# Kernel optimization log

Measured on AMD Instinct MI355X. Metric: run time of the kernel, lower is better.

Reference implementation:

```python
import jax, jax.numpy as jnp
import numpy as np

MACRO_CURVE_ORDER = 3
MAX_ACTION_LEN = 24
NUM_CURVES = 8
VOCAB = 361
NUM_LAYERS = 6
HID = 32


def setup_inputs() -> dict:
    key = jax.random.key(0)
    ks = iter(jax.random.split(key, 32))
    B, N_PART, P, CTX = 4096, 100, 64, 64

    def lin(k, din, dout):
        k1, k2 = jax.random.split(k)
        s = 1.0 / np.sqrt(din)
        return (jax.random.uniform(k1, (din, dout), jnp.float32, -s, s),
                jax.random.uniform(k2, (dout,), jnp.float32, -s, s))

    fc1_w, fc1_b = lin(next(ks), P, 256)
    fc2_w, fc2_b = lin(next(ks), 256, 256)
    fc3_w, fc3_b = lin(next(ks), CTX + 256, 512)
    fc4_w, fc4_b = lin(next(ks), 512, 256)
    fc5_w, fc5_b = lin(next(ks), 256, 128)
    fc6_w, fc6_b = lin(next(ks), 128, 32)
    fc10_w, fc10_b = lin(next(ks), HID, VOCAB)

    s = 1.0 / np.sqrt(HID)
    lstm_wih = jax.random.uniform(next(ks), (NUM_LAYERS, HID, 4 * HID), jnp.float32, -s, s)
    lstm_whh = jax.random.uniform(next(ks), (NUM_LAYERS, HID, 4 * HID), jnp.float32, -s, s)
    lstm_bih = jax.random.uniform(next(ks), (NUM_LAYERS, 4 * HID), jnp.float32, -s, s)
    lstm_bhh = jax.random.uniform(next(ks), (NUM_LAYERS, 4 * HID), jnp.float32, -s, s)

    return {
        "c": jax.random.normal(next(ks), (B, CTX), jnp.float32),
        "x": jax.random.normal(next(ks), (B, N_PART * P), jnp.float32),
        "hidden": jnp.zeros((NUM_LAYERS, B, HID), jnp.float32),
        "cell": jnp.zeros((NUM_LAYERS, B, HID), jnp.float32),
        "fc1_w": fc1_w, "fc1_b": fc1_b, "fc2_w": fc2_w, "fc2_b": fc2_b,
        "fc3_w": fc3_w, "fc3_b": fc3_b, "fc4_w": fc4_w, "fc4_b": fc4_b,
        "fc5_w": fc5_w, "fc5_b": fc5_b, "fc6_w": fc6_w, "fc6_b": fc6_b,
        "lstm_wih": lstm_wih, "lstm_whh": lstm_whh,
        "lstm_bih": lstm_bih, "lstm_bhh": lstm_bhh,
        "fc10_w": fc10_w, "fc10_b": fc10_b,
        "particle_size": P,
    }


def _lstm_stack(x, h, c, wih, whh, bih, bhh):
    """One time step through 6 stacked LSTM layers (PyTorch cell math)."""
    hs, cs = [], []
    inp = x
    for l in range(NUM_LAYERS):
        gates = inp @ wih[l] + bih[l] + h[l] @ whh[l] + bhh[l]  # (B, 4*HID)
        i, f, g, o = jnp.split(gates, 4, axis=-1)
        i, f, o = jax.nn.sigmoid(i), jax.nn.sigmoid(f), jax.nn.sigmoid(o)
        g = jnp.tanh(g)
        c_new = f * c[l] + i * g
        h_new = o * jnp.tanh(c_new)
        hs.append(h_new)
        cs.append(c_new)
        inp = h_new
    return inp, jnp.stack(hs), jnp.stack(cs)


def reference(c, x, hidden, cell, fc1_w, fc1_b, fc2_w, fc2_b, fc3_w, fc3_b,
              fc4_w, fc4_b, fc5_w, fc5_b, fc6_w, fc6_b,
              lstm_wih, lstm_whh, lstm_bih, lstm_bhh, fc10_w, fc10_b,
              particle_size):
    B = x.shape[0]
    # Belief (particle) encoder with mean pooling.
    xp = x.reshape(B, -1, particle_size)
    xp = jax.nn.relu(xp @ fc1_w + fc1_b)
    xp = jax.nn.relu(xp @ fc2_w + fc2_b)
    xp = xp.mean(axis=-2)  # (B, 256)
    z = jnp.concatenate([c, xp], axis=-1)
    z = jax.nn.relu(z @ fc3_w + fc3_b)
    z = jax.nn.relu(z @ fc4_w + fc4_b)
    z = jax.nn.relu(z @ fc5_w + fc5_b)
    z = jax.nn.relu(z @ fc6_w + fc6_b)  # (B, 32)

    def step(carry, _):
        xt, h, cst = carry
        xt, h, cst = _lstm_stack(xt, h, cst, lstm_wih, lstm_whh, lstm_bih, lstm_bhh)
        logits = xt @ fc10_w + fc10_b  # (B, VOCAB)
        idx = jax.lax.top_k(logits, NUM_CURVES)[1]  # (B, NUM_CURVES)
        return (xt, h, cst), idx

    (_, _, _), idxs = jax.lax.scan(step, (z, hidden, cell), None, length=MAX_ACTION_LEN)
    # (T, B, K) -> (B, T*K)
    preds = jnp.transpose(idxs, (1, 0, 2)).reshape(B, MAX_ACTION_LEN * NUM_CURVES)
    return preds
```

## Files before the change

### kernel.cpp

```cpp
#include <hip/hip_runtime.h>
#include <math.h>

#define BATCH 4096
#define NPART 100
#define PSZ   64

__global__ __launch_bounds__(256, 3) void k_encoder(
    const float* __restrict__ x,
    const float* __restrict__ w1, const float* __restrict__ b1,
    const float* __restrict__ w2, const float* __restrict__ b2,
    float* __restrict__ xp)
{
    __shared__ float h1[32][256];
    const int tid = threadIdx.x;
    const int b   = blockIdx.x;

    float w1c[64];
    #pragma unroll
    for (int k = 0; k < 64; ++k) w1c[k] = w1[k * 256 + tid];
    const float b1j = b1[tid];

    const int tx = tid & 31;
    const int ty = tid >> 5;
    const float4 b2a = *(const float4*)&b2[tx * 8];
    const float4 b2b = *(const float4*)&b2[tx * 8 + 4];
    float msum[8] = {0.f,0.f,0.f,0.f,0.f,0.f,0.f,0.f};

    const float* xb  = x + (size_t)b * (NPART * PSZ);
    const float* w2p = w2 + tx * 8;

    for (int ch = 0; ch < 4; ++ch) {
        const int rbase = ch * 32;
        const int rows  = (rbase + 32 <= NPART) ? 32 : (NPART - rbase);

        #pragma unroll 2
        for (int p = 0; p < rows; ++p) {
            const float4* xr = (const float4*)(xb + (rbase + p) * 64);
            float acc = b1j;
            #pragma unroll
            for (int kq = 0; kq < 16; ++kq) {
                const float4 xv = xr[kq];
                acc = fmaf(xv.x, w1c[4*kq+0], acc);
                acc = fmaf(xv.y, w1c[4*kq+1], acc);
                acc = fmaf(xv.z, w1c[4*kq+2], acc);
                acc = fmaf(xv.w, w1c[4*kq+3], acc);
            }
            h1[p][tid] = fmaxf(acc, 0.f);
        }
        __syncthreads();

        float acc[4][8];
        #pragma unroll
        for (int r = 0; r < 4; ++r)
            #pragma unroll
            for (int q = 0; q < 8; ++q) acc[r][q] = 0.f;

        #pragma unroll 2
        for (int k0 = 0; k0 < 256; k0 += 4) {
            float4 bv0[4], bv1[4];
            #pragma unroll
            for (int kk = 0; kk < 4; ++kk) {
                bv0[kk] = *(const float4*)(w2p + (k0 + kk) * 256);
                bv1[kk] = *(const float4*)(w2p + (k0 + kk) * 256 + 4);
            }
            float4 av[4];
            #pragma unroll
            for (int r = 0; r < 4; ++r)
                av[r] = *(const float4*)&h1[ty * 4 + r][k0];
            #pragma unroll
            for (int r = 0; r < 4; ++r) {
                const float a0 = av[r].x, a1 = av[r].y, a2 = av[r].z, a3 = av[r].w;
                acc[r][0] = fmaf(a0, bv0[0].x, fmaf(a1, bv0[1].x, fmaf(a2, bv0[2].x, fmaf(a3, bv0[3].x, acc[r][0]))));
                acc[r][1] = fmaf(a0, bv0[0].y, fmaf(a1, bv0[1].y, fmaf(a2, bv0[2].y, fmaf(a3, bv0[3].y, acc[r][1]))));
                acc[r][2] = fmaf(a0, bv0[0].z, fmaf(a1, bv0[1].z, fmaf(a2, bv0[2].z, fmaf(a3, bv0[3].z, acc[r][2]))));
                acc[r][3] = fmaf(a0, bv0[0].w, fmaf(a1, bv0[1].w, fmaf(a2, bv0[2].w, fmaf(a3, bv0[3].w, acc[r][3]))));
                acc[r][4] = fmaf(a0, bv1[0].x, fmaf(a1, bv1[1].x, fmaf(a2, bv1[2].x, fmaf(a3, bv1[3].x, acc[r][4]))));
                acc[r][5] = fmaf(a0, bv1[0].y, fmaf(a1, bv1[1].y, fmaf(a2, bv1[2].y, fmaf(a3, bv1[3].y, acc[r][5]))));
                acc[r][6] = fmaf(a0, bv1[0].z, fmaf(a1, bv1[1].z, fmaf(a2, bv1[2].z, fmaf(a3, bv1[3].z, acc[r][6]))));
                acc[r][7] = fmaf(a0, bv1[0].w, fmaf(a1, bv1[1].w, fmaf(a2, bv1[2].w, fmaf(a3, bv1[3].w, acc[r][7]))));
            }
        }

        #pragma unroll
        for (int r = 0; r < 4; ++r) {
            const int grow = rbase + ty * 4 + r;
            if (grow < NPART) {
                msum[0] += fmaxf(acc[r][0] + b2a.x, 0.f);
                msum[1] += fmaxf(acc[r][1] + b2a.y, 0.f);
                msum[2] += fmaxf(acc[r][2] + b2a.z, 0.f);
                msum[3] += fmaxf(acc[r][3] + b2a.w, 0.f);
                msum[4] += fmaxf(acc[r][4] + b2b.x, 0.f);
                msum[5] += fmaxf(acc[r][5] + b2b.y, 0.f);
                msum[6] += fmaxf(acc[r][6] + b2b.z, 0.f);
                msum[7] += fmaxf(acc[r][7] + b2b.w, 0.f);
            }
        }
        __syncthreads();
    }

    float* red = &h1[0][0];
    #pragma unroll
    for (int q = 0; q < 8; ++q) red[ty * 256 + tx * 8 + q] = msum[q];
    __syncthreads();
    float s = 0.f;
    #pragma unroll
    for (int g = 0; g < 8; ++g) s += red[g * 256 + tid];
    xp[(size_t)b * 256 + tid] = s / 100.0f;
}

__global__ __launch_bounds__(256) void k_mlp(
    const float* __restrict__ cin, const float* __restrict__ xp,
    const float* __restrict__ w3, const float* __restrict__ b3,
    const float* __restrict__ w4, const float* __restrict__ b4,
    const float* __restrict__ w5, const float* __restrict__ b5,
    const float* __restrict__ w6, const float* __restrict__ b6,
    float* __restrict__ z)
{
    __shared__ float in0[8][320];
    __shared__ float h3[8][512];
    __shared__ float h4[8][256];
    __shared__ float h5[8][128];
    const int tid  = threadIdx.x;
    const int row0 = blockIdx.x * 8;

    for (int i = tid; i < 8 * 16; i += 256) {
        int r = i >> 4, q = i & 15;
        *(float4*)&in0[r][q * 4] = *(const float4*)&cin[(size_t)(row0 + r) * 64 + q * 4];
    }
    for (int i = tid; i < 8 * 64; i += 256) {
        int r = i >> 6, q = i & 63;
        *(float4*)&in0[r][64 + q * 4] = *(const float4*)&xp[(size_t)(row0 + r) * 256 + q * 4];
    }
    __syncthreads();

    {
        float a0[8], a1[8];
        #pragma unroll
        for (int r = 0; r < 8; ++r) { a0[r] = 0.f; a1[r] = 0.f; }
        const int c0 = tid, c1 = tid + 256;
        for (int kq = 0; kq < 80; ++kq) {
            const int k0 = kq * 4;
            float wa0 = w3[(k0+0)*512 + c0], wa1 = w3[(k0+1)*512 + c0];
            float wa2 = w3[(k0+2)*512 + c0], wa3 = w3[(k0+3)*512 + c0];
            float wb0 = w3[(k0+0)*512 + c1], wb1 = w3[(k0+1)*512 + c1];
            float wb2 = w3[(k0+2)*512 + c1], wb3 = w3[(k0+3)*512 + c1];
            #pragma unroll
            for (int r = 0; r < 8; ++r) {
                const float4 a = *(const float4*)&in0[r][k0];
                a0[r] = fmaf(a.x, wa0, fmaf(a.y, wa1, fmaf(a.z, wa2, fmaf(a.w, wa3, a0[r]))));
                a1[r] = fmaf(a.x, wb0, fmaf(a.y, wb1, fmaf(a.z, wb2, fmaf(a.w, wb3, a1[r]))));
            }
        }
        const float bb0 = b3[c0], bb1 = b3[c1];
        #pragma unroll
        for (int r = 0; r < 8; ++r) {
            h3[r][c0] = fmaxf(a0[r] + bb0, 0.f);
            h3[r][c1] = fmaxf(a1[r] + bb1, 0.f);
        }
    }
    __syncthreads();

    {
        float ac[8];
        #pragma unroll
        for (int r = 0; r < 8; ++r) ac[r] = 0.f;
        for (int kq = 0; kq < 128; ++kq) {
            const int k0 = kq * 4;
            float w0 = w4[(k0+0)*256 + tid], w1v = w4[(k0+1)*256 + tid];
            float w2v = w4[(k0+2)*256 + tid], w3v = w4[(k0+3)*256 + tid];
            #pragma unroll
            for (int r = 0; r < 8; ++r) {
                const float4 a = *(const float4*)&h3[r][k0];
                ac[r] = fmaf(a.x, w0, fmaf(a.y, w1v, fmaf(a.z, w2v, fmaf(a.w, w3v, ac[r]))));
            }
        }
        const float bb = b4[tid];
        #pragma unroll
        for (int r = 0; r < 8; ++r) h4[r][tid] = fmaxf(ac[r] + bb, 0.f);
    }
    __syncthreads();

    {
        const int c5 = tid & 127, half = tid >> 7;
        float ac[4];
        #pragma unroll
        for (int r = 0; r < 4; ++r) ac[r] = 0.f;
        for (int kq = 0; kq < 64; ++kq) {
            const int k0 = kq * 4;
            float w0 = w5[(k0+0)*128 + c5], w1v = w5[(k0+1)*128 + c5];
            float w2v = w5[(k0+2)*128 + c5], w3v = w5[(k0+3)*128 + c5];
            #pragma unroll
            for (int r = 0; r < 4; ++r) {
                const float4 a = *(const float4*)&h4[half * 4 + r][k0];
                ac[r] = fmaf(a.x, w0, fmaf(a.y, w1v, fmaf(a.z, w2v, fmaf(a.w, w3v, ac[r]))));
            }
        }
        const float bb = b5[c5];
        #pragma unroll
        for (int r = 0; r < 4; ++r) h5[half * 4 + r][c5] = fmaxf(ac[r] + bb, 0.f);
    }
    __syncthreads();

    {
        const int c6 = tid & 31, r = tid >> 5;
        float ac = 0.f;
        for (int kq = 0; kq < 32; ++kq) {
            const int k0 = kq * 4;
            float w0 = w6[(k0+0)*32 + c6], w1v = w6[(k0+1)*32 + c6];
            float w2v = w6[(k0+2)*32 + c6], w3v = w6[(k0+3)*32 + c6];
            const float4 a = *(const float4*)&h5[r][k0];
            ac = fmaf(a.x, w0, fmaf(a.y, w1v, fmaf(a.z, w2v, fmaf(a.w, w3v, ac))));
        }
        z[(size_t)(row0 + r) * 32 + c6] = fmaxf(ac + b6[c6], 0.f);
    }
}

__global__ __launch_bounds__(256) void k_lstm(
    const float* __restrict__ z,
    const float* __restrict__ hid0, const float* __restrict__ cel0,
    const float* __restrict__ wih, const float* __restrict__ whh,
    const float* __restrict__ bih, const float* __restrict__ bhh,
    const float* __restrict__ w10, const float* __restrict__ b10,
    int* __restrict__ out)
{
    __shared__ float xs[8][32];
    __shared__ float hs[6][8][32];
    __shared__ float cs[6][8][32];
    __shared__ float gates[8][128];
    __shared__ float logits[8][361];
    const int tid  = threadIdx.x;
    const int row0 = blockIdx.x * 8;

    for (int i = tid; i < 8 * 32; i += 256) xs[0][i] = z[(size_t)row0 * 32 + i];
    for (int i = tid; i < 6 * 8 * 32; i += 256) {
        int l = i >> 8, rj = i & 255;
        (&hs[0][0][0])[i] = hid0[(size_t)l * BATCH * 32 + (size_t)row0 * 32 + rj];
        (&cs[0][0][0])[i] = cel0[(size_t)l * BATCH * 32 + (size_t)row0 * 32 + rj];
    }
    __syncthreads();

    const int g  = tid & 127, rg = tid >> 7;
    const int jc = tid & 31,  jr = tid >> 5;
    const int wv = tid >> 6,  lane = tid & 63;

    for (int t = 0; t < 24; ++t) {
        for (int l = 0; l < 6; ++l) {
            const float* inp = (l == 0) ? ((t == 0) ? &xs[0][0] : &hs[5][0][0])
                                        : &hs[l - 1][0][0];
            const float* WI = wih + (size_t)l * 32 * 128;
            const float* WH = whh + (size_t)l * 32 * 128;
            const float bsum = bih[l * 128 + g] + bhh[l * 128 + g];
            float acc[4] = {bsum, bsum, bsum, bsum};
            #pragma unroll
            for (int k = 0; k < 32; k += 4) {
                float wi0 = WI[(k+0)*128 + g], wi1 = WI[(k+1)*128 + g];
                float wi2 = WI[(k+2)*128 + g], wi3 = WI[(k+3)*128 + g];
                float wh0 = WH[(k+0)*128 + g], wh1 = WH[(k+1)*128 + g];
                float wh2 = WH[(k+2)*128 + g], wh3 = WH[(k+3)*128 + g];
                #pragma unroll
                for (int rr = 0; rr < 4; ++rr) {
                    const int r = rg * 4 + rr;
                    const float4 ai = *(const float4*)&inp[r * 32 + k];
                    const float4 ah = *(const float4*)&hs[l][r][k];
                    acc[rr] = fmaf(ai.x, wi0, acc[rr]); acc[rr] = fmaf(ai.y, wi1, acc[rr]);
                    acc[rr] = fmaf(ai.z, wi2, acc[rr]); acc[rr] = fmaf(ai.w, wi3, acc[rr]);
                    acc[rr] = fmaf(ah.x, wh0, acc[rr]); acc[rr] = fmaf(ah.y, wh1, acc[rr]);
                    acc[rr] = fmaf(ah.z, wh2, acc[rr]); acc[rr] = fmaf(ah.w, wh3, acc[rr]);
                }
            }
            #pragma unroll
            for (int rr = 0; rr < 4; ++rr) gates[rg * 4 + rr][g] = acc[rr];
            __syncthreads();

            {
                const float gi = gates[jr][jc],      gf = gates[jr][32 + jc];
                const float gg = gates[jr][64 + jc], go = gates[jr][96 + jc];
                const float i_ = 1.f / (1.f + expf(-gi));
                const float f_ = 1.f / (1.f + expf(-gf));
                const float o_ = 1.f / (1.f + expf(-go));
                const float g_ = tanhf(gg);
                const float cn = f_ * cs[l][jr][jc] + i_ * g_;
                cs[l][jr][jc] = cn;
                hs[l][jr][jc] = o_ * tanhf(cn);
            }
            __syncthreads();
        }

        #pragma unroll
        for (int pass = 0; pass < 2; ++pass) {
            const int v = tid + pass * 256;
            if (v < 361) {
                const float bb = b10[v];
                float a8[8];
                #pragma unroll
                for (int r = 0; r < 8; ++r) a8[r] = bb;
                #pragma unroll
                for (int k = 0; k < 32; k += 4) {
                    float w0 = w10[(k+0)*361 + v], w1v = w10[(k+1)*361 + v];
                    float w2v = w10[(k+2)*361 + v], w3v = w10[(k+3)*361 + v];
                    #pragma unroll
                    for (int r = 0; r < 8; ++r) {
                        const float4 a = *(const float4*)&hs[5][r][k];
                        a8[r] = fmaf(a.x, w0, fmaf(a.y, w1v, fmaf(a.z, w2v, fmaf(a.w, w3v, a8[r]))));
                    }
                }
                #pragma unroll
                for (int r = 0; r < 8; ++r) logits[r][v] = a8[r];
            }
        }
        __syncthreads();

        for (int rr = 0; rr < 2; ++rr) {
            const int r = wv * 2 + rr;
            float val[6];
            #pragma unroll
            for (int s = 0; s < 6; ++s) {
                const int v = lane + 64 * s;
                val[s] = (v < 361) ? logits[r][v] : -3.4e38f;
            }
            unsigned msk = 0x3Fu;
            const int rowg = row0 + r;
            for (int sel = 0; sel < 8; ++sel) {
                float bv = -3.4e38f; int bi = 0x7FFFFFFF;
                #pragma unroll
                for (int s = 0; s < 6; ++s) {
                    if (msk & (1u << s)) {
                        const float v2 = val[s]; const int i2 = lane + 64 * s;
                        if (v2 > bv || (v2 == bv && i2 < bi)) { bv = v2; bi = i2; }
                    }
                }
                #pragma unroll
                for (int off = 32; off >= 1; off >>= 1) {
                    const float ov = __shfl_xor(bv, off, 64);
                    const int   oi = __shfl_xor(bi, off, 64);
                    if (ov > bv || (ov == bv && oi < bi)) { bv = ov; bi = oi; }
                }
                if ((bi & 63) == lane) msk &= ~(1u << (bi >> 6));
                if (lane == 0) out[(size_t)rowg * 192 + t * 8 + sel] = bi;
            }
        }
        __syncthreads();
    }
}

extern "C" void kernel_launch(void* const* d_in, const int* in_sizes, int n_in,
                              void* d_out, int out_size, void* d_ws, size_t ws_size,
                              hipStream_t stream) {
    const float* cin  = (const float*)d_in[0];
    const float* x    = (const float*)d_in[1];
    const float* hid0 = (const float*)d_in[2];
    const float* cel0 = (const float*)d_in[3];
    const float* w1 = (const float*)d_in[4];  const float* b1 = (const float*)d_in[5];
    const float* w2 = (const float*)d_in[6];  const float* b2 = (const float*)d_in[7];
    const float* w3 = (const float*)d_in[8];  const float* b3 = (const float*)d_in[9];
    const float* w4 = (const float*)d_in[10]; const float* b4 = (const float*)d_in[11];
    const float* w5 = (const float*)d_in[12]; const float* b5 = (const float*)d_in[13];
    const float* w6 = (const float*)d_in[14]; const float* b6 = (const float*)d_in[15];
    const float* wih = (const float*)d_in[16]; const float* whh = (const float*)d_in[17];
    const float* bih = (const float*)d_in[18]; const float* bhh = (const float*)d_in[19];
    const float* w10 = (const float*)d_in[20]; const float* b10 = (const float*)d_in[21];

    float* xp = (float*)d_ws;
    float* zz = xp + (size_t)BATCH * 256;
    int*   out = (int*)d_out;

    k_encoder<<<BATCH, 256, 0, stream>>>(x, w1, b1, w2, b2, xp);
    k_mlp<<<BATCH / 8, 256, 0, stream>>>(cin, xp, w3, b3, w4, b4, w5, b5, w6, b6, zz);
    k_lstm<<<BATCH / 8, 256, 0, stream>>>(zz, hid0, cel0, wih, whh, bih, bhh, w10, b10, out);
}
```

Measured before the change: 2.628 ms.

## Restructure particle encoder into register-tiled fc1/fc2 with staged x and shuffle reduction

Rewrites the encoder kernel so fc1 is computed as a register-tiled GEMM. The x chunk is staged in padded shared memory and w1 is streamed from global like w2, replacing the per-thread 64-register w1 cache and the serial per-row dot products. It also changes thread mapping so each wave owns 64 output columns, pads shared rows to avoid bank conflicts, and replaces the shared-memory mean reduction with wave shuffles. The aim is higher FMA throughput and fewer global x reads per thread. In exchange, w1 is reloaded from global for every chunk, and the minimum-occupancy launch bound is dropped.

```diff
diff --git a/kernel.cpp b/kernel.cpp
--- a/kernel.cpp
+++ b/kernel.cpp
@@ -5,107 +5,145 @@
 #define NPART 100
 #define PSZ   64
 
-__global__ __launch_bounds__(256, 3) void k_encoder(
+__device__ __forceinline__ void fma4(float4& d, const float s, const float4 v) {
+    d.x = fmaf(s, v.x, d.x); d.y = fmaf(s, v.y, d.y);
+    d.z = fmaf(s, v.z, d.z); d.w = fmaf(s, v.w, d.w);
+}
+__device__ __forceinline__ float4 addrelu4(const float4 a, const float4 b) {
+    return make_float4(fmaxf(a.x + b.x, 0.f), fmaxf(a.y + b.y, 0.f),
+                       fmaxf(a.z + b.z, 0.f), fmaxf(a.w + b.w, 0.f));
+}
+
+template<int NRR, int ROWS>
+__device__ __forceinline__ void enc_chunk(
+    const float* __restrict__ xb, const int rbase,
+    const float* __restrict__ w1c, const float* __restrict__ w2c,
+    float* __restrict__ h1s, float* __restrict__ xss,
+    const int tid, const int rg, const int col0,
+    const float4 b1a, const float4 b1b, const float4 b2a, const float4 b2b,
+    float* msum)
+{
+    for (int i = tid; i < ROWS * 16; i += 256) {
+        const int r = i >> 4, q = (i & 15) * 4;
+        *(float4*)&xss[r * 68 + q] = *(const float4*)(xb + (size_t)(rbase + r) * 64 + q);
+    }
+    __syncthreads();
+
+    float4 a0[NRR], a1[NRR];
+    #pragma unroll
+    for (int rr = 0; rr < NRR; ++rr) {
+        a0[rr] = make_float4(0.f, 0.f, 0.f, 0.f);
+        a1[rr] = make_float4(0.f, 0.f, 0.f, 0.f);
+    }
+    #pragma unroll 2
+    for (int k0 = 0; k0 < 64; k0 += 4) {
+        float4 bva[4], bvb[4];
+        #pragma unroll
+        for (int kk = 0; kk < 4; ++kk) {
+            bva[kk] = *(const float4*)(w1c + (k0 + kk) * 256);
+            bvb[kk] = *(const float4*)(w1c + (k0 + kk) * 256 + 4);
+        }
+        #pragma unroll
+        for (int rr = 0; rr < NRR; ++rr) {
+            const float4 a = *(const float4*)&xss[(rg + 8 * rr) * 68 + k0];
+            fma4(a0[rr], a.x, bva[0]); fma4(a0[rr], a.y, bva[1]);
+            fma4(a0[rr], a.z, bva[2]); fma4(a0[rr], a.w, bva[3]);
+            fma4(a1[rr], a.x, bvb[0]); fma4(a1[rr], a.y, bvb[1]);
+            fma4(a1[rr], a.z, bvb[2]); fma4(a1[rr], a.w, bvb[3]);
+        }
+    }
+    #pragma unroll
+    for (int rr = 0; rr < NRR; ++rr) {
+        const int r = rg + 8 * rr;
+        *(float4*)&h1s[r * 260 + col0]     = addrelu4(a0[rr], b1a);
+        *(float4*)&h1s[r * 260 + col0 + 4] = addrelu4(a1[rr], b1b);
+    }
+    __syncthreads();
+
+    float4 c0[NRR], c1[NRR];
+    #pragma unroll
+    for (int rr = 0; rr < NRR; ++rr) {
+        c0[rr] = make_float4(0.f, 0.f, 0.f, 0.f);
+        c1[rr] = make_float4(0.f, 0.f, 0.f, 0.f);
+    }
+    #pragma unroll 2
+    for (int k0 = 0; k0 < 256; k0 += 4) {
+        float4 bva[4], bvb[4];
+        #pragma unroll
+        for (int kk = 0; kk < 4; ++kk) {
+            bva[kk] = *(const float4*)(w2c + (k0 + kk) * 256);
+            bvb[kk] = *(const float4*)(w2c + (k0 + kk) * 256 + 4);
+        }
+        #pragma unroll
+        for (int rr = 0; rr < NRR; ++rr) {
+            const float4 a = *(const float4*)&h1s[(rg + 8 * rr) * 260 + k0];
+            fma4(c0[rr], a.x, bva[0]); fma4(c0[rr], a.y, bva[1]);
+            fma4(c0[rr], a.z, bva[2]); fma4(c0[rr], a.w, bva[3]);
+            fma4(c1[rr], a.x, bvb[0]); fma4(c1[rr], a.y, bvb[1]);
+            fma4(c1[rr], a.z, bvb[2]); fma4(c1[rr], a.w, bvb[3]);
+        }
+    }
+    #pragma unroll
+    for (int rr = 0; rr < NRR; ++rr) {
+        if (NRR == 4 || rg < 4) {
+            msum[0] += fmaxf(c0[rr].x + b2a.x, 0.f);
+            msum[1] += fmaxf(c0[rr].y + b2a.y, 0.f);
+            msum[2] += fmaxf(c0[rr].z + b2a.z, 0.f);
+            msum[3] += fmaxf(c0[rr].w + b2a.w, 0.f);
+            msum[4] += fmaxf(c1[rr].x + b2b.x, 0.f);
+            msum[5] += fmaxf(c1[rr].y + b2b.y, 0.f);
+            msum[6] += fmaxf(c1[rr].z + b2b.z, 0.f);
+            msum[7] += fmaxf(c1[rr].w + b2b.w, 0.f);
+        }
+    }
+    __syncthreads();
+}
+
+__global__ __launch_bounds__(256) void k_encoder(
     const float* __restrict__ x,
     const float* __restrict__ w1, const float* __restrict__ b1,
     const float* __restrict__ w2, const float* __restrict__ b2,
     float* __restrict__ xp)
 {
-    __shared__ float h1[32][256];
-    const int tid = threadIdx.x;
-    const int b   = blockIdx.x;
-
-    float w1c[64];
+    __shared__ __align__(16) float h1s[32 * 260];
+    __shared__ __align__(16) float xss[32 * 68];
+    const int tid  = threadIdx.x;
+    const int b    = blockIdx.x;
+    const int lane = tid & 63;
+    const int wv   = tid >> 6;
+    const int cg   = lane & 7;
+    const int rg   = lane >> 3;
+    const int col0 = wv * 64 + cg * 8;
+
+    const float* xb  = x + (size_t)b * (NPART * PSZ);
+    const float* w1c = w1 + col0;
+    const float* w2c = w2 + col0;
+    const float4 b1a = *(const float4*)&b1[col0];
+    const float4 b1b = *(const float4*)&b1[col0 + 4];
+    const float4 b2a = *(const float4*)&b2[col0];
+    const float4 b2b = *(const float4*)&b2[col0 + 4];
+
+    float msum[8] = {0.f,0.f,0.f,0.f,0.f,0.f,0.f,0.f};
+
+    enc_chunk<4,32>(xb,  0, w1c, w2c, h1s, xss, tid, rg, col0, b1a, b1b, b2a, b2b, msum);
+    enc_chunk<4,32>(xb, 32, w1c, w2c, h1s, xss, tid, rg, col0, b1a, b1b, b2a, b2b, msum);
+    enc_chunk<4,32>(xb, 64, w1c, w2c, h1s, xss, tid, rg, col0, b1a, b1b, b2a, b2b, msum);
+    enc_chunk<1, 4>(xb, 96, w1c, w2c, h1s, xss, tid, rg, col0, b1a, b1b, b2a, b2b, msum);
+
     #pragma unroll
-    for (int k = 0; k < 64; ++k) w1c[k] = w1[k * 256 + tid];
-    const float b1j = b1[tid];
-
-    const int tx = tid & 31;
-    const int ty = tid >> 5;
-    const float4 b2a = *(const float4*)&b2[tx * 8];
-    const float4 b2b = *(const float4*)&b2[tx * 8 + 4];
-    float msum[8] = {0.f,0.f,0.f,0.f,0.f,0.f,0.f,0.f};
-
-    const float* xb  = x + (size_t)b * (NPART * PSZ);
-    const float* w2p = w2 + tx * 8;
-
-    for (int ch = 0; ch < 4; ++ch) {
-        const int rbase = ch * 32;
-        const int rows  = (rbase + 32 <= NPART) ? 32 : (NPART - rbase);
-
-        #pragma unroll 2
-        for (int p = 0; p < rows; ++p) {
-            const float4* xr = (const float4*)(xb + (rbase + p) * 64);
-            float acc = b1j;
-            #pragma unroll
-            for (int kq = 0; kq < 16; ++kq) {
-                const float4 xv = xr[kq];
-                acc = fmaf(xv.x, w1c[4*kq+0], acc);
-                acc = fmaf(xv.y, w1c[4*kq+1], acc);
-                acc = fmaf(xv.z, w1c[4*kq+2], acc);
-                acc = fmaf(xv.w, w1c[4*kq+3], acc);
-            }
-            h1[p][tid] = fmaxf(acc, 0.f);
-        }
-        __syncthreads();
-
-        float acc[4][8];
-        #pragma unroll
-        for (int r = 0; r < 4; ++r)
-            #pragma unroll
-            for (int q = 0; q < 8; ++q) acc[r][q] = 0.f;
-
-        #pragma unroll 2
-        for (int k0 = 0; k0 < 256; k0 += 4) {
-            float4 bv0[4], bv1[4];
-            #pragma unroll
-            for (int kk = 0; kk < 4; ++kk) {
-                bv0[kk] = *(const float4*)(w2p + (k0 + kk) * 256);
-                bv1[kk] = *(const float4*)(w2p + (k0 + kk) * 256 + 4);
-            }
-            float4 av[4];
-            #pragma unroll
-            for (int r = 0; r < 4; ++r)
-                av[r] = *(const float4*)&h1[ty * 4 + r][k0];
-            #pragma unroll
-            for (int r = 0; r < 4; ++r) {
-                const float a0 = av[r].x, a1 = av[r].y, a2 = av[r].z, a3 = av[r].w;
-                acc[r][0] = fmaf(a0, bv0[0].x, fmaf(a1, bv0[1].x, fmaf(a2, bv0[2].x, fmaf(a3, bv0[3].x, acc[r][0]))));
-                acc[r][1] = fmaf(a0, bv0[0].y, fmaf(a1, bv0[1].y, fmaf(a2, bv0[2].y, fmaf(a3, bv0[3].y, acc[r][1]))));
-                acc[r][2] = fmaf(a0, bv0[0].z, fmaf(a1, bv0[1].z, fmaf(a2, bv0[2].z, fmaf(a3, bv0[3].z, acc[r][2]))));
-                acc[r][3] = fmaf(a0, bv0[0].w, fmaf(a1, bv0[1].w, fmaf(a2, bv0[2].w, fmaf(a3, bv0[3].w, acc[r][3]))));
-                acc[r][4] = fmaf(a0, bv1[0].x, fmaf(a1, bv1[1].x, fmaf(a2, bv1[2].x, fmaf(a3, bv1[3].x, acc[r][4]))));
-                acc[r][5] = fmaf(a0, bv1[0].y, fmaf(a1, bv1[1].y, fmaf(a2, bv1[2].y, fmaf(a3, bv1[3].y, acc[r][5]))));
-                acc[r][6] = fmaf(a0, bv1[0].z, fmaf(a1, bv1[1].z, fmaf(a2, bv1[2].z, fmaf(a3, bv1[3].z, acc[r][6]))));
-                acc[r][7] = fmaf(a0, bv1[0].w, fmaf(a1, bv1[1].w, fmaf(a2, bv1[2].w, fmaf(a3, bv1[3].w, acc[r][7]))));
-            }
-        }
-
-        #pragma unroll
-        for (int r = 0; r < 4; ++r) {
-            const int grow = rbase + ty * 4 + r;
-            if (grow < NPART) {
-                msum[0] += fmaxf(acc[r][0] + b2a.x, 0.f);
-                msum[1] += fmaxf(acc[r][1] + b2a.y, 0.f);
-                msum[2] += fmaxf(acc[r][2] + b2a.z, 0.f);
-                msum[3] += fmaxf(acc[r][3] + b2a.w, 0.f);
-                msum[4] += fmaxf(acc[r][4] + b2b.x, 0.f);
-                msum[5] += fmaxf(acc[r][5] + b2b.y, 0.f);
-                msum[6] += fmaxf(acc[r][6] + b2b.z, 0.f);
-                msum[7] += fmaxf(acc[r][7] + b2b.w, 0.f);
-            }
-        }
-        __syncthreads();
-    }
-
-    float* red = &h1[0][0];
-    #pragma unroll
-    for (int q = 0; q < 8; ++q) red[ty * 256 + tx * 8 + q] = msum[q];
-    __syncthreads();
-    float s = 0.f;
-    #pragma unroll
-    for (int g = 0; g < 8; ++g) s += red[g * 256 + tid];
-    xp[(size_t)b * 256 + tid] = s / 100.0f;
+    for (int q = 0; q < 8; ++q) {
+        msum[q] += __shfl_xor(msum[q], 8, 64);
+        msum[q] += __shfl_xor(msum[q], 16, 64);
+        msum[q] += __shfl_xor(msum[q], 32, 64);
+    }
+    if (rg == 0) {
+        float4 o0 = make_float4(msum[0] / 100.f, msum[1] / 100.f,
+                                msum[2] / 100.f, msum[3] / 100.f);
+        float4 o1 = make_float4(msum[4] / 100.f, msum[5] / 100.f,
+                                msum[6] / 100.f, msum[7] / 100.f);
+        *(float4*)&xp[(size_t)b * 256 + col0]     = o0;
+        *(float4*)&xp[(size_t)b * 256 + col0 + 4] = o1;
+    }
 }
 
 __global__ __launch_bounds__(256) void k_mlp(
```

New measurement: 2.310 ms. 12.1% less time.
